# Performance work log

Hardware: AMD Instinct MI355X
Metric: run time of the kernel (lower is better)

Reference implementation:

```python
import jax, jax.numpy as jnp
import numpy as np

B, S, D = 2048, 200, 128  # batch, history length, embedding dim
H = 64                    # attention_units[0]

def setup_inputs() -> dict:
    key = jax.random.key(0)
    k1, k2, k3, k4, k5 = jax.random.split(key, 5)
    return {
        "target_item": jax.random.normal(k1, (B, D), dtype=jnp.float32),
        "history_sequence": jax.random.normal(k2, (B, S, D), dtype=jnp.float32),
        "mask": jax.random.randint(k3, (B, S), 0, 2, dtype=jnp.int32),
        "W1": jax.random.normal(k4, (4 * D, H), dtype=jnp.float32) * (1.0 / np.sqrt(4 * D)),
        "b1": jnp.zeros((H,), dtype=jnp.float32),
        "W2": jax.random.normal(k5, (H, 1), dtype=jnp.float32) * (1.0 / np.sqrt(H)),
        "b2": jnp.zeros((1,), dtype=jnp.float32),
    }

def reference(target_item, history_sequence, mask, W1, b1, W2, b2):
    b, s, d = history_sequence.shape
    t = jnp.broadcast_to(target_item[:, None, :], (b, s, d))  # [B,S,D]
    # concat(target, history, diff, product) -> [B,S,4D]
    x = jnp.concatenate(
        [t, history_sequence, t - history_sequence, t * history_sequence], axis=-1)
    h = jax.nn.relu(x @ W1 + b1)          # [B,S,H]
    w = (h @ W2 + b2)[..., 0]             # [B,S]
    m = mask.astype(w.dtype)
    w = w * m                              # zero out padded positions (pre-softmax, as in source)
    w = w + (-1e9) * (1.0 - m)             # mask for softmax
    w = jax.nn.softmax(w, axis=-1)
    return jnp.einsum('bs,bsd->bd', w, history_sequence)  # [B,D]
```

## Files before the change

### kernel.cpp

```cpp
#include <hip/hip_runtime.h>
#include <hip/hip_bf16.h>

typedef __attribute__((ext_vector_type(8))) short bf16x8;
typedef __attribute__((ext_vector_type(4))) float f32x4;

#define B_ 2048
#define S_ 200
#define D_ 128
#define H_ 64
#define LOG2E 1.44269504f
#define TR 8
#define TB 4096

#define WS_AC 0u
#define WS_WB 32768u
#define WS_MT 65536u

static __device__ __forceinline__ short f2bf_hw(float f) {
    return (short)__builtin_bit_cast(unsigned short, __float2bfloat16(f));
}

static __device__ __forceinline__ void gload16(const void* g, void* l) {
    __builtin_amdgcn_global_load_lds(
        (const __attribute__((address_space(1))) unsigned int*)g,
        (__attribute__((address_space(3))) unsigned int*)l, 16, 0, 0);
}

__global__ __launch_bounds__(128)
void prep_fold(const float* __restrict__ W1, char* __restrict__ ws)
{
    const int n = blockIdx.x;
    const int k = threadIdx.x;
    float a = W1[k * H_ + n];
    float b = W1[(128 + k) * H_ + n];
    float c = W1[(256 + k) * H_ + n];
    float d = W1[(384 + k) * H_ + n];
    ((float*)(ws + WS_AC))[n * 128 + k] = a + c;
    char* img = ws + WS_WB;
    const int sw = (n & 7) << 4;
    const int kk = k >> 3, e2 = (k & 7) * 2;
    *(short*)(img + n * 512 + ((kk * 16) ^ sw) + e2)          = f2bf_hw(b - c);
    *(short*)(img + n * 512 + (((16 + kk) * 16) ^ sw) + e2)   = f2bf_hw(d);
}

__global__ __launch_bounds__(256)
void prep_ta(const float* __restrict__ tgt, const float* __restrict__ b1,
             char* __restrict__ ws)
{
    __shared__ float tl[4][128];
    const int tid = threadIdx.x;
    const int b0 = blockIdx.x * 4;
    if (tid < 128) {
        int bb = tid >> 5, q = tid & 31;
        *(float4*)&tl[bb][q * 4] = ((const float4*)(tgt + (size_t)(b0 + bb) * D_))[q];
    }
    __syncthreads();
    const int n = tid & 63, bb = tid >> 6;
    const float* ac = (const float*)(ws + WS_AC) + n * 128;
    float s = 0.f;
    #pragma unroll 8
    for (int d = 0; d < 128; ++d) s = fmaf(tl[bb][d], ac[d], s);
    ((float*)(ws + WS_MT + (size_t)(b0 + bb) * 2048u + 512u))[n] = s + b1[n];
}

__global__ __launch_bounds__(256)
void mask_build(const int* __restrict__ mask, const float* __restrict__ tgt,
                char* __restrict__ ws)
{
    const int lane = threadIdx.x & 63;
    const int wv   = threadIdx.x >> 6;
    const int b    = blockIdx.x * 4 + wv;
    const int* mp  = mask + (size_t)b * S_;
    char* mt = ws + WS_MT + (size_t)b * 2048u;
    int* lst = (int*)(mt + 1024);
    int cnt = 0, last = 0;
    #pragma unroll
    for (int c = 0; c < 4; ++c) {
        int s = c * 64 + lane;
        int m = (s < S_) ? mp[s] : 0;
        unsigned long long bal = __ballot(m != 0);
        if (m) lst[cnt + __builtin_popcountll(bal & ((1ull << lane) - 1ull))] = s;
        if (bal) last = c * 64 + (63 - __builtin_clzll(bal));
        cnt += __builtin_popcountll(bal);
    }
    int uni = 0;
    if (cnt == 0) { uni = 1; cnt = S_; }
    for (int p = cnt + lane; p < 208; p += 64) lst[p] = uni ? (S_ - 1) : last;
    if (uni)
        for (int p = lane; p < S_; p += 64) lst[p] = p;
    if (lane == 0) *(int*)(mt + 768) = cnt | (uni << 16);
    if (lane < 32) ((float4*)mt)[lane] = ((const float4*)(tgt + (size_t)b * D_))[lane];
}

__global__ __launch_bounds__(256) __attribute__((amdgpu_waves_per_eu(2, 2)))
void din_fused(const float* __restrict__ hist, const float* __restrict__ W2,
               const char* __restrict__ ws, float* __restrict__ out)
{
    __shared__ __align__(16) char L[73728];
    const int tid  = threadIdx.x;
    const int lane = tid & 63;
    const int wv   = tid >> 6;
    const int b    = blockIdx.x * 4 + wv;
    const int lo   = lane & 15;
    const int hi   = lane >> 4;
    char* Lm = L + 32768 + wv * 10240;
    char* B0 = Lm + 2048;
    char* B1 = Lm + 6144;

    f32x4 w2v[4];
    #pragma unroll
    for (int ng = 0; ng < 4; ++ng) {
        f32x4 wl = *(const f32x4*)(W2 + ng * 16 + hi * 4);
        w2v[ng] = (f32x4){wl[0] * LOG2E, wl[1] * LOG2E, wl[2] * LOG2E, wl[3] * LOG2E};
    }

    {
        const char* wsrc = ws + WS_WB + wv * 8192 + (size_t)lane * 16u;
        #pragma unroll
        for (int i = 0; i < 8; ++i)
            gload16(wsrc + i * 1024, L + wv * 8192 + i * 1024);
        const char* msrc = ws + WS_MT + (size_t)b * 2048u + (size_t)lane * 16u;
        gload16(msrc,        Lm);
        gload16(msrc + 1024, Lm + 1024);
    }
    asm volatile("s_waitcnt vmcnt(0)" ::: "memory");
    __syncthreads();

    const int cw  = *(const int*)(Lm + 768);
    const int cnt = cw & 0xffff;
    const int uni = cw >> 16;
    int nt = (cnt + TR - 1) / TR; if (nt < 2) nt = 2;
    const int* ll = (const int*)(Lm + 1024);

    f32x4 tav[4];
    #pragma unroll
    for (int ng = 0; ng < 4; ++ng)
        tav[ng] = *(const f32x4*)(Lm + 512 + (ng * 16 + hi * 4) * 4);

    int abase[4], akoff[8];
    #pragma unroll
    for (int ng = 0; ng < 4; ++ng) abase[ng] = (ng * 16 + lo) * 512;
    #pragma unroll
    for (int ks = 0; ks < 8; ++ks) akoff[ks] = (ks * 64 + hi * 16) ^ ((lo & 7) << 4);
    const int rb   = ((lo & 7) * 512 + hi * 32) ^ ((lo & 7) << 4);
    const int toff = hi * 32;

    const char* hb = (const char*)hist + (size_t)b * (S_ * D_ * 4);
    const int cp = (lane & 31) * 16;
    const int h5 = lane >> 5;

    {
        #pragma unroll
        for (int i = 0; i < 4; ++i) {
            int r = 2 * i + h5;
            gload16(hb + (size_t)ll[r] * 512 + (cp ^ ((r & 7) << 4)), B0 + i * 1024);
        }
        #pragma unroll
        for (int i = 0; i < 4; ++i) {
            int r = 2 * i + h5;
            gload16(hb + (size_t)ll[8 + r] * 512 + (cp ^ ((r & 7) << 4)), B1 + i * 1024);
        }
    }

    float o[4][8];
    #pragma unroll
    for (int ks = 0; ks < 4; ++ks)
        #pragma unroll
        for (int e = 0; e < 8; ++e) o[ks][e] = 0.f;
    float l = 0.f, mx = -1e30f;

    auto compt = [&](int t, char* buf, int nxt) {
        int r[4];
        if (nxt >= 0) {
            #pragma unroll
            for (int i = 0; i < 4; ++i) r[i] = ll[nxt * TR + 2 * i + h5];
        }
        f32x4 acc[4];
        #pragma unroll
        for (int ng = 0; ng < 4; ++ng) acc[ng] = (f32x4){0.f, 0.f, 0.f, 0.f};
        #pragma unroll
        for (int ks = 0; ks < 4; ++ks) {
            int o4 = rb + ks * 128;
            f32x4 h0  = *(const f32x4*)(buf + o4);
            f32x4 h1  = *(const f32x4*)(buf + (o4 ^ 16));
            f32x4 tp0 = *(const f32x4*)(Lm + ks * 128 + toff);
            f32x4 tp1 = *(const f32x4*)(Lm + ks * 128 + toff + 16);
            bf16x8 bh, bt;
            #pragma unroll
            for (int e = 0; e < 4; ++e) {
                bh[e]     = f2bf_hw(h0[e]);
                bh[e + 4] = f2bf_hw(h1[e]);
                bt[e]     = f2bf_hw(tp0[e] * h0[e]);
                bt[e + 4] = f2bf_hw(tp1[e] * h1[e]);
            }
            #pragma unroll
            for (int ng = 0; ng < 4; ++ng) {
                bf16x8 af = *(const bf16x8*)(L + abase[ng] + akoff[ks]);
                acc[ng] = __builtin_amdgcn_mfma_f32_16x16x32_bf16(af, bh, acc[ng], 0, 0, 0);
            }
            #pragma unroll
            for (int ng = 0; ng < 4; ++ng) {
                bf16x8 af = *(const bf16x8*)(L + abase[ng] + akoff[ks + 4]);
                acc[ng] = __builtin_amdgcn_mfma_f32_16x16x32_bf16(af, bt, acc[ng], 0, 0, 0);
            }
        }
        float s0 = 0.f, s1 = 0.f, s2 = 0.f, s3 = 0.f;
        #pragma unroll
        for (int e = 0; e < 4; ++e) {
            s0 = fmaf(fmaxf(acc[0][e] + tav[0][e], 0.f), w2v[0][e], s0);
            s1 = fmaf(fmaxf(acc[1][e] + tav[1][e], 0.f), w2v[1][e], s1);
            s2 = fmaf(fmaxf(acc[2][e] + tav[2][e], 0.f), w2v[2][e], s2);
            s3 = fmaf(fmaxf(acc[3][e] + tav[3][e], 0.f), w2v[3][e], s3);
        }
        float sum = (s0 + s1) + (s2 + s3);
        sum += __shfl_xor(sum, 16);
        sum += __shfl_xor(sum, 32);
        const bool valid = (t * TR + lo < cnt) && (lo < TR);
        float lg = uni ? (valid ? 0.f : -1e30f) : (valid ? sum : -1e30f);
        float tm = lg;
        tm = fmaxf(tm, __shfl_xor(tm, 1));
        tm = fmaxf(tm, __shfl_xor(tm, 2));
        tm = fmaxf(tm, __shfl_xor(tm, 4));
        tm = fmaxf(tm, __shfl_xor(tm, 8));
        if (tm > mx + 11.5f) {
            float rsc = exp2f(mx - tm);
            #pragma unroll
            for (int ks = 0; ks < 4; ++ks)
                #pragma unroll
                for (int e = 0; e < 8; ++e) o[ks][e] *= rsc;
            l *= rsc;
            mx = tm;
        }
        float p = valid ? exp2f(lg - mx) : 0.f;
        l += p;
        #pragma unroll
        for (int ks = 0; ks < 4; ++ks) {
            int o4 = rb + ks * 128;
            f32x4 h0 = *(const f32x4*)(buf + o4);
            f32x4 h1 = *(const f32x4*)(buf + (o4 ^ 16));
            o[ks][0] = fmaf(p, h0[0], o[ks][0]);
            o[ks][1] = fmaf(p, h0[1], o[ks][1]);
            o[ks][2] = fmaf(p, h0[2], o[ks][2]);
            o[ks][3] = fmaf(p, h0[3], o[ks][3]);
            o[ks][4] = fmaf(p, h1[0], o[ks][4]);
            o[ks][5] = fmaf(p, h1[1], o[ks][5]);
            o[ks][6] = fmaf(p, h1[2], o[ks][6]);
            o[ks][7] = fmaf(p, h1[3], o[ks][7]);
        }
        asm volatile("s_waitcnt lgkmcnt(0)" ::: "memory");
        __builtin_amdgcn_sched_barrier(0);
        if (nxt >= 0) {
            #pragma unroll
            for (int i = 0; i < 4; ++i)
                gload16(hb + (size_t)r[i] * 512 + (cp ^ (((2 * i + h5) & 7) << 4)),
                        buf + i * 1024);
        }
    };

    #pragma unroll 1
    for (int t = 0; t < nt; ++t) {
        char* buf = (t & 1) ? B1 : B0;
        if (t + 1 < nt) { asm volatile("s_waitcnt vmcnt(4)" ::: "memory"); }
        else            { asm volatile("s_waitcnt vmcnt(0)" ::: "memory"); }
        __builtin_amdgcn_sched_barrier(0);
        compt(t, buf, (t + 2 < nt) ? t + 2 : -1);
    }

    #pragma unroll
    for (int ks = 0; ks < 4; ++ks)
        #pragma unroll
        for (int e = 0; e < 8; ++e) {
            float v = o[ks][e];
            v += __shfl_xor(v, 1);
            v += __shfl_xor(v, 2);
            v += __shfl_xor(v, 4);
            v += __shfl_xor(v, 8);
            o[ks][e] = v;
        }
    l += __shfl_xor(l, 1);
    l += __shfl_xor(l, 2);
    l += __shfl_xor(l, 4);
    l += __shfl_xor(l, 8);

    const float inv = 1.0f / l;
    if (lo == 0) {
        float* op = out + (size_t)b * D_ + hi * 8;
        #pragma unroll
        for (int ks = 0; ks < 4; ++ks) {
            *(f32x4*)(op + ks * 32)     = (f32x4){o[ks][0] * inv, o[ks][1] * inv,
                                                  o[ks][2] * inv, o[ks][3] * inv};
            *(f32x4*)(op + ks * 32 + 4) = (f32x4){o[ks][4] * inv, o[ks][5] * inv,
                                                  o[ks][6] * inv, o[ks][7] * inv};
        }
    }
}

extern "C" void kernel_launch(void* const* d_in, const int* in_sizes, int n_in,
                              void* d_out, int out_size, void* d_ws, size_t ws_size,
                              hipStream_t stream) {
    const float* tgt  = (const float*)d_in[0];
    const float* hist = (const float*)d_in[1];
    const int*   mask = (const int*)d_in[2];
    const float* W1   = (const float*)d_in[3];
    const float* b1   = (const float*)d_in[4];
    const float* W2   = (const float*)d_in[5];
    const float* b2   = (const float*)d_in[6];
    (void)b2;
    float* out = (float*)d_out;
    char* ws = (char*)d_ws;

    prep_fold<<<64, 128, 0, stream>>>(W1, ws);
    prep_ta<<<B_ / 4, 256, 0, stream>>>(tgt, b1, ws);
    mask_build<<<B_ / 4, 256, 0, stream>>>(mask, tgt, ws);
    din_fused<<<B_ / 4, 256, 0, stream>>>(hist, W2, ws, out);
}
```

Measured before the change: 57.72 us.

## Use 16-row tiles with triple-buffered history staging and register-resident weights

Each tile now holds 16 history rows instead of 8, so every lane in a 16-wide MFMA column carries a valid row. History loads move from double to triple buffering. Tile data is read into registers once, so the buffer can be refilled early and is not read a second time for the weighted sum. The history-half bf16 weight fragments and the target slices are kept in registers for the whole kernel. The cost is 139 KB of LDS per block and one wave per EU, which lowers occupancy and leans on deeper prefetch to hide memory latency.

```diff
diff --git a/kernel.cpp b/kernel.cpp
--- a/kernel.cpp
+++ b/kernel.cpp
@@ -9,8 +9,8 @@
 #define D_ 128
 #define H_ 64
 #define LOG2E 1.44269504f
-#define TR 8
-#define TB 4096
+#define TR 16
+#define TB 8192
 
 #define WS_AC 0u
 #define WS_WB 32768u
@@ -39,8 +39,8 @@
     char* img = ws + WS_WB;
     const int sw = (n & 7) << 4;
     const int kk = k >> 3, e2 = (k & 7) * 2;
-    *(short*)(img + n * 512 + ((kk * 16) ^ sw) + e2)          = f2bf_hw(b - c);
-    *(short*)(img + n * 512 + (((16 + kk) * 16) ^ sw) + e2)   = f2bf_hw(d);
+    *(short*)(img + n * 512 + ((kk * 16) ^ sw) + e2)        = f2bf_hw(b - c);
+    *(short*)(img + n * 512 + (((16 + kk) * 16) ^ sw) + e2) = f2bf_hw(d);
 }
 
 __global__ __launch_bounds__(256)
@@ -92,20 +92,18 @@
     if (lane < 32) ((float4*)mt)[lane] = ((const float4*)(tgt + (size_t)b * D_))[lane];
 }
 
-__global__ __launch_bounds__(256) __attribute__((amdgpu_waves_per_eu(2, 2)))
+__global__ __launch_bounds__(256) __attribute__((amdgpu_waves_per_eu(1, 1)))
 void din_fused(const float* __restrict__ hist, const float* __restrict__ W2,
                const char* __restrict__ ws, float* __restrict__ out)
 {
-    __shared__ __align__(16) char L[73728];
+    __shared__ __align__(16) char L[139264];
     const int tid  = threadIdx.x;
     const int lane = tid & 63;
     const int wv   = tid >> 6;
     const int b    = blockIdx.x * 4 + wv;
     const int lo   = lane & 15;
     const int hi   = lane >> 4;
-    char* Lm = L + 32768 + wv * 10240;
-    char* B0 = Lm + 2048;
-    char* B1 = Lm + 6144;
+    char* Lm = L + 32768 + wv * 26624;
 
     f32x4 w2v[4];
     #pragma unroll
@@ -129,38 +127,51 @@
     const int cw  = *(const int*)(Lm + 768);
     const int cnt = cw & 0xffff;
     const int uni = cw >> 16;
-    int nt = (cnt + TR - 1) / TR; if (nt < 2) nt = 2;
+    const int nt  = (cnt + 15) >> 4;
     const int* ll = (const int*)(Lm + 1024);
 
     f32x4 tav[4];
     #pragma unroll
     for (int ng = 0; ng < 4; ++ng)
         tav[ng] = *(const f32x4*)(Lm + 512 + (ng * 16 + hi * 4) * 4);
+    f32x4 tp0[4], tp1[4];
+    #pragma unroll
+    for (int ks = 0; ks < 4; ++ks) {
+        tp0[ks] = *(const f32x4*)(Lm + ks * 128 + hi * 32);
+        tp1[ks] = *(const f32x4*)(Lm + ks * 128 + hi * 32 + 16);
+    }
 
     int abase[4], akoff[8];
     #pragma unroll
     for (int ng = 0; ng < 4; ++ng) abase[ng] = (ng * 16 + lo) * 512;
     #pragma unroll
     for (int ks = 0; ks < 8; ++ks) akoff[ks] = (ks * 64 + hi * 16) ^ ((lo & 7) << 4);
-    const int rb   = ((lo & 7) * 512 + hi * 32) ^ ((lo & 7) << 4);
-    const int toff = hi * 32;
+    bf16x8 bfH[4][4];
+    #pragma unroll
+    for (int ks = 0; ks < 4; ++ks)
+        #pragma unroll
+        for (int ng = 0; ng < 4; ++ng)
+            bfH[ks][ng] = *(const bf16x8*)(L + abase[ng] + akoff[ks]);
+
+    const int rb = (lo * 512 + hi * 32) ^ ((lo & 7) << 4);
+    char* BB0 = Lm + 2048;
+    char* BB1 = Lm + 2048 + TB;
+    char* BB2 = Lm + 2048 + 2 * TB;
 
     const char* hb = (const char*)hist + (size_t)b * (S_ * D_ * 4);
     const int cp = (lane & 31) * 16;
     const int h5 = lane >> 5;
-
-    {
-        #pragma unroll
-        for (int i = 0; i < 4; ++i) {
+    auto stage = [&](int t, char* bufp) {
+        #pragma unroll
+        for (int i = 0; i < 8; ++i) {
             int r = 2 * i + h5;
-            gload16(hb + (size_t)ll[r] * 512 + (cp ^ ((r & 7) << 4)), B0 + i * 1024);
-        }
-        #pragma unroll
-        for (int i = 0; i < 4; ++i) {
-            int r = 2 * i + h5;
-            gload16(hb + (size_t)ll[8 + r] * 512 + (cp ^ ((r & 7) << 4)), B1 + i * 1024);
-        }
-    }
+            int rr = ll[t * 16 + r];
+            gload16(hb + (size_t)rr * 512 + (cp ^ ((r & 7) << 4)), bufp + i * 1024);
+        }
+    };
+    stage(0, BB0);
+    stage(nt > 1 ? 1 : 0, BB1);
+    stage(nt > 2 ? 2 : nt - 1, BB2);
 
     float o[4][8];
     #pragma unroll
@@ -169,39 +180,44 @@
         for (int e = 0; e < 8; ++e) o[ks][e] = 0.f;
     float l = 0.f, mx = -1e30f;
 
-    auto compt = [&](int t, char* buf, int nxt) {
-        int r[4];
-        if (nxt >= 0) {
-            #pragma unroll
-            for (int i = 0; i < 4; ++i) r[i] = ll[nxt * TR + 2 * i + h5];
-        }
-        f32x4 acc[4];
-        #pragma unroll
-        for (int ng = 0; ng < 4; ++ng) acc[ng] = (f32x4){0.f, 0.f, 0.f, 0.f};
+    #pragma unroll 1
+    for (int t = 0; t < nt; ++t) {
+        char* buf = (t % 3 == 0) ? BB0 : (t % 3 == 1) ? BB1 : BB2;
+        asm volatile("s_waitcnt vmcnt(16)" ::: "memory");
+        __builtin_amdgcn_sched_barrier(0);
+        f32x4 h0[4], h1[4];
         #pragma unroll
         for (int ks = 0; ks < 4; ++ks) {
             int o4 = rb + ks * 128;
-            f32x4 h0  = *(const f32x4*)(buf + o4);
-            f32x4 h1  = *(const f32x4*)(buf + (o4 ^ 16));
-            f32x4 tp0 = *(const f32x4*)(Lm + ks * 128 + toff);
-            f32x4 tp1 = *(const f32x4*)(Lm + ks * 128 + toff + 16);
+            h0[ks] = *(const f32x4*)(buf + o4);
+            h1[ks] = *(const f32x4*)(buf + (o4 ^ 16));
+        }
+        asm volatile("s_waitcnt lgkmcnt(0)" ::: "memory");
+        __builtin_amdgcn_sched_barrier(0);
+        if (t + 1 < nt) {
+            int ts = t + 3; if (ts > nt - 1) ts = nt - 1;
+            stage(ts, buf);
+        }
+        f32x4 acc[4];
+        #pragma unroll
+        for (int ng = 0; ng < 4; ++ng) acc[ng] = (f32x4){0.f, 0.f, 0.f, 0.f};
+        #pragma unroll
+        for (int ks = 0; ks < 4; ++ks) {
             bf16x8 bh, bt;
             #pragma unroll
             for (int e = 0; e < 4; ++e) {
-                bh[e]     = f2bf_hw(h0[e]);
-                bh[e + 4] = f2bf_hw(h1[e]);
-                bt[e]     = f2bf_hw(tp0[e] * h0[e]);
-                bt[e + 4] = f2bf_hw(tp1[e] * h1[e]);
+                bh[e]     = f2bf_hw(h0[ks][e]);
+                bh[e + 4] = f2bf_hw(h1[ks][e]);
+                bt[e]     = f2bf_hw(tp0[ks][e] * h0[ks][e]);
+                bt[e + 4] = f2bf_hw(tp1[ks][e] * h1[ks][e]);
             }
             #pragma unroll
-            for (int ng = 0; ng < 4; ++ng) {
-                bf16x8 af = *(const bf16x8*)(L + abase[ng] + akoff[ks]);
-                acc[ng] = __builtin_amdgcn_mfma_f32_16x16x32_bf16(af, bh, acc[ng], 0, 0, 0);
-            }
+            for (int ng = 0; ng < 4; ++ng)
+                acc[ng] = __builtin_amdgcn_mfma_f32_16x16x32_bf16(bfH[ks][ng], bh, acc[ng], 0, 0, 0);
             #pragma unroll
             for (int ng = 0; ng < 4; ++ng) {
-                bf16x8 af = *(const bf16x8*)(L + abase[ng] + akoff[ks + 4]);
-                acc[ng] = __builtin_amdgcn_mfma_f32_16x16x32_bf16(af, bt, acc[ng], 0, 0, 0);
+                bf16x8 afd = *(const bf16x8*)(L + abase[ng] + akoff[ks + 4]);
+                acc[ng] = __builtin_amdgcn_mfma_f32_16x16x32_bf16(afd, bt, acc[ng], 0, 0, 0);
             }
         }
         float s0 = 0.f, s1 = 0.f, s2 = 0.f, s3 = 0.f;
@@ -215,7 +231,7 @@
         float sum = (s0 + s1) + (s2 + s3);
         sum += __shfl_xor(sum, 16);
         sum += __shfl_xor(sum, 32);
-        const bool valid = (t * TR + lo < cnt) && (lo < TR);
+        const bool valid = (t * 16 + lo) < cnt;
         float lg = uni ? (valid ? 0.f : -1e30f) : (valid ? sum : -1e30f);
         float tm = lg;
         tm = fmaxf(tm, __shfl_xor(tm, 1));
@@ -235,35 +251,15 @@
         l += p;
         #pragma unroll
         for (int ks = 0; ks < 4; ++ks) {
-            int o4 = rb + ks * 128;
-            f32x4 h0 = *(const f32x4*)(buf + o4);
-            f32x4 h1 = *(const f32x4*)(buf + (o4 ^ 16));
-            o[ks][0] = fmaf(p, h0[0], o[ks][0]);
-            o[ks][1] = fmaf(p, h0[1], o[ks][1]);
-            o[ks][2] = fmaf(p, h0[2], o[ks][2]);
-            o[ks][3] = fmaf(p, h0[3], o[ks][3]);
-            o[ks][4] = fmaf(p, h1[0], o[ks][4]);
-            o[ks][5] = fmaf(p, h1[1], o[ks][5]);
-            o[ks][6] = fmaf(p, h1[2], o[ks][6]);
-            o[ks][7] = fmaf(p, h1[3], o[ks][7]);
-        }
-        asm volatile("s_waitcnt lgkmcnt(0)" ::: "memory");
-        __builtin_amdgcn_sched_barrier(0);
-        if (nxt >= 0) {
-            #pragma unroll
-            for (int i = 0; i < 4; ++i)
-                gload16(hb + (size_t)r[i] * 512 + (cp ^ (((2 * i + h5) & 7) << 4)),
-                        buf + i * 1024);
-        }
-    };
-
-    #pragma unroll 1
-    for (int t = 0; t < nt; ++t) {
-        char* buf = (t & 1) ? B1 : B0;
-        if (t + 1 < nt) { asm volatile("s_waitcnt vmcnt(4)" ::: "memory"); }
-        else            { asm volatile("s_waitcnt vmcnt(0)" ::: "memory"); }
-        __builtin_amdgcn_sched_barrier(0);
-        compt(t, buf, (t + 2 < nt) ? t + 2 : -1);
+            o[ks][0] = fmaf(p, h0[ks][0], o[ks][0]);
+            o[ks][1] = fmaf(p, h0[ks][1], o[ks][1]);
+            o[ks][2] = fmaf(p, h0[ks][2], o[ks][2]);
+            o[ks][3] = fmaf(p, h0[ks][3], o[ks][3]);
+            o[ks][4] = fmaf(p, h1[ks][0], o[ks][4]);
+            o[ks][5] = fmaf(p, h1[ks][1], o[ks][5]);
+            o[ks][6] = fmaf(p, h1[ks][2], o[ks][6]);
+            o[ks][7] = fmaf(p, h1[ks][3], o[ks][7]);
+        }
     }
 
     #pragma unroll
```

Result: faster. 56.39 us (-2.3%).
